# Performance work log

Hardware: AMD Instinct MI355X
Metric: run time of the kernel (lower is better)

## Reference

```python
import jax, jax.numpy as jnp
import numpy as np

N_NODES = 20000
N_EDGES = 320000
N_GRAPHS = 256
D = 256
L = 4
EPS = 1e-5


def setup_inputs() -> dict:
    key = jax.random.key(0)
    ks = jax.random.split(key, 20)
    x = jax.random.normal(ks[0], (N_NODES, D), dtype=jnp.float32)
    edge_index = jax.random.randint(ks[1], (2, N_EDGES), 0, N_NODES, dtype=jnp.int64)
    batch = jnp.sort(jax.random.randint(ks[2], (N_NODES,), 0, N_GRAPHS, dtype=jnp.int64))
    s = 1.0 / np.sqrt(D)
    Wl = jax.random.uniform(ks[3], (L, D, D), jnp.float32, -s, s)
    bl = jax.random.uniform(ks[4], (L, D), jnp.float32, -s, s)
    Wr = jax.random.uniform(ks[5], (L, D, D), jnp.float32, -s, s)
    gamma = jnp.ones((L, D), jnp.float32)
    beta = jnp.zeros((L, D), jnp.float32)
    fc1_w = jax.random.uniform(ks[6], (D, 128), jnp.float32, -s, s)
    fc1_b = jax.random.uniform(ks[7], (128,), jnp.float32, -s, s)
    s2 = 1.0 / np.sqrt(128)
    fc2_w = jax.random.uniform(ks[8], (128, 64), jnp.float32, -s2, s2)
    fc2_b = jax.random.uniform(ks[9], (64,), jnp.float32, -s2, s2)
    s3 = 1.0 / np.sqrt(64)
    fc3_w = jax.random.uniform(ks[10], (64, 10), jnp.float32, -s3, s3)
    fc3_b = jax.random.uniform(ks[11], (10,), jnp.float32, -s3, s3)
    return dict(x=x, edge_index=edge_index, batch=batch, Wl=Wl, bl=bl, Wr=Wr,
                gamma=gamma, beta=beta, fc1_w=fc1_w, fc1_b=fc1_b,
                fc2_w=fc2_w, fc2_b=fc2_b, fc3_w=fc3_w, fc3_b=fc3_b)


def reference(x, edge_index, batch, Wl, bl, Wr, gamma, beta,
              fc1_w, fc1_b, fc2_w, fc2_b, fc3_w, fc3_b):
    src, dst = edge_index[0], edge_index[1]
    # in-degree for mean aggregation (zero-degree nodes -> 0 aggregate)
    deg = jax.ops.segment_sum(jnp.ones((src.shape[0],), x.dtype), dst, num_segments=N_NODES)
    inv_deg = jnp.where(deg > 0, 1.0 / jnp.maximum(deg, 1.0), 0.0)[:, None]
    for i in range(L):
        # SAGEConv: mean-aggregate neighbors, then lin_l(agg) + lin_r(x)
        agg = jax.ops.segment_sum(x[src], dst, num_segments=N_NODES) * inv_deg
        h = agg @ Wl[i] + bl[i] + x @ Wr[i]
        # BatchNorm (training mode: biased batch statistics over nodes)
        mu = jnp.mean(h, axis=0)
        var = jnp.mean(jnp.square(h - mu), axis=0)
        h = (h - mu) * jax.lax.rsqrt(var + EPS) * gamma[i] + beta[i]
        x = jax.nn.relu(h)
    # global_mean_pool over graphs
    cnt = jax.ops.segment_sum(jnp.ones((N_NODES,), x.dtype), batch, num_segments=N_GRAPHS)
    g = jax.ops.segment_sum(x, batch, num_segments=N_GRAPHS) / jnp.maximum(cnt, 1.0)[:, None]
    # MLP classifier: 256 -> 128 -> 64 -> 10
    g = jax.nn.relu(g @ fc1_w + fc1_b)
    g = jax.nn.relu(g @ fc2_w + fc2_b)
    return g @ fc3_w + fc3_b
```

## Files before the change

### kernel.cpp

```cpp
#include <hip/hip_runtime.h>
#include <hip/hip_bf16.h>

#define NN 20000
#define NE 320000
#define NG 256
#define DD 256
#define NL 4
#define NBKT 79
#define BM 80
#define NBLK 250

typedef __attribute__((ext_vector_type(8))) short short8;
typedef __attribute__((ext_vector_type(4))) float float4_t;

__device__ __forceinline__ int ld_idx(const int* __restrict__ p, int i, int f64) {
    return f64 ? p[2 * i] : p[i];
}

__device__ __forceinline__ float bf2f(ushort u) {
    return __uint_as_float(((unsigned)u) << 16);
}

__device__ __forceinline__ ushort f2bf(float f) {
    __hip_bfloat16 b = __float2bfloat16(f);
    return *(ushort*)&b;
}


__global__ void k_init(const int* __restrict__ ei, const int* __restrict__ batch,
                       const ushort* __restrict__ x, int* __restrict__ flags,
                       int* __restrict__ deg) {
    int gid = blockIdx.x * 256 + threadIdx.x;
    for (int i = gid; i < NN; i += gridDim.x * 256) deg[i] = 0;
    if (blockIdx.x == 0) {
        __shared__ int cnt0, cnt1, weird;
        int t = threadIdx.x;
        if (t == 0) { cnt0 = 0; cnt1 = 0; weird = 0; }
        __syncthreads();
        for (int tt = t; tt < 512; tt += 256) {
            if (ei[2 * tt + 1] != 0) atomicAdd(&cnt0, 1);
            int i = tt * 9;
            if (batch[2 * i + 1] != 0) atomicAdd(&cnt1, 1);
#pragma unroll
            for (int j = 0; j < 16; j++) {
                ushort v = x[tt * 16 + j];
                if (((v >> 7) & 0xFF) >= 0xC0) atomicAdd(&weird, 1);
            }
        }
        __syncthreads();
        if (t == 0) {
            flags[0] = (cnt0 == 0) ? 1 : 0;
            flags[1] = (cnt1 == 0) ? 1 : 0;
            flags[2] = (weird == 0) ? 1 : 0;
        }
    }
}


#define POFF_BL   0
#define POFF_GA   1024
#define POFF_BE   2048
#define POFF_F1W  3072
#define POFF_F1B  35840
#define POFF_F2W  35968
#define POFF_F2B  44160
#define POFF_F3W  44224
#define POFF_F3B  44864
#define PTOT      44874

#define NB_CVT8   2500
#define NB_FRAG   128
#define NB_CVTP   176
#define NB_DEG    1250
#define NB_GST    79
#define B_FRAG    (NB_CVT8)
#define B_CVTP    (B_FRAG + NB_FRAG)
#define B_DEG     (B_CVTP + NB_CVTP)
#define B_GST     (B_DEG + NB_DEG)
#define NB_PREP   (B_GST + NB_GST)


__global__ __launch_bounds__(256) void k_prep(
    const void* __restrict__ x_in, const void* __restrict__ WL,
    const void* __restrict__ WR, const int* __restrict__ ei,
    const int* __restrict__ batch,
    const void* s0, const void* s1, const void* s2, const void* s3,
    const void* s4, const void* s5, const void* s6, const void* s7, const void* s8,
    ushort* __restrict__ xcan, ushort* __restrict__ wtL, ushort* __restrict__ wtR,
    ushort* __restrict__ pcan, int* __restrict__ deg, int* __restrict__ gstart,
    const int* __restrict__ fl) {
    int blk = blockIdx.x;
    int t = threadIdx.x;
    if (blk < B_FRAG) {
        int i = blk * 256 + t;
        if (fl[2]) {
            *(int4*)(xcan + (size_t)i * 8) = ((const int4*)x_in)[i];
        } else {
            const float* f = (const float*)x_in + (size_t)i * 8;
            ushort ov[8];
#pragma unroll
            for (int d = 0; d < 8; d++) ov[d] = f2bf(f[d]);
            *(int4*)(xcan + (size_t)i * 8) = *(int4*)ov;
        }
    } else if (blk < B_CVTP) {
        __shared__ ushort T[64][65];
        int bid = blk - B_FRAG;
        int lm = bid >> 4;
        int tile = bid & 15;
        int tk = (tile >> 2) * 64, tn = (tile & 3) * 64;
        const void* W = (lm >= 4) ? WR : WL;
        ushort* Wt = (lm >= 4) ? wtR : wtL;
        size_t base = (size_t)(lm & 3) << 16;
        int f32 = !fl[2];
#pragma unroll
        for (int i = 0; i < 16; i++) {
            int flat = t + i * 256;
            int r = flat >> 6, c = flat & 63;
            size_t src = base + (size_t)(tk + r) * 256 + tn + c;
            ushort v = f32 ? f2bf(((const float*)W)[src]) : ((const ushort*)W)[src];
            T[c][r] = v;
        }
        __syncthreads();
#pragma unroll
        for (int i = 0; i < 2; i++) {
            int slot = t + i * 256;
            int f = slot >> 6;
            int lane = slot & 63;
            int ln = (f >> 1) * 16 + (lane & 15);
            int lk = (f & 1) * 32 + ((lane >> 4) << 3);
            int gfblk = ((tn + ln) >> 4) * 8 + ((tk + lk) >> 5);
            ushort tmp[8];
#pragma unroll
            for (int j = 0; j < 8; j++) tmp[j] = T[ln][lk + j];
            *(int4*)(Wt + base + (size_t)gfblk * 512 + lane * 8) = *(int4*)tmp;
        }
    } else if (blk < B_DEG) {
        int i = (blk - B_CVTP) * 256 + t;
        if (i >= PTOT) return;
        const int offs[10] = {POFF_BL, POFF_GA, POFF_BE, POFF_F1W, POFF_F1B,
                              POFF_F2W, POFF_F2B, POFF_F3W, POFF_F3B, PTOT};
        const void* srcs[9] = {s0, s1, s2, s3, s4, s5, s6, s7, s8};
        int seg = 0;
#pragma unroll
        for (int k = 1; k < 9; k++) if (i >= offs[k]) seg = k;
        int local = i - offs[seg];
        if (fl[2]) pcan[i] = ((const ushort*)srcs[seg])[local];
        else       pcan[i] = f2bf(((const float*)srcs[seg])[local]);
    } else if (blk < B_GST) {
        int e = (blk - B_DEG) * 256 + t;
        if (e < NE) {
            int src = ld_idx(ei, e, fl[0]);
            int dst = ld_idx(ei, NE + e, fl[0]);
            if ((unsigned)dst < NN && (unsigned)src < NN) atomicAdd(&deg[dst], 1);
        }
    } else {
        int i = (blk - B_GST) * 256 + t;
        if (i >= NN) return;
        int b = ld_idx(batch, i, fl[1]);
        int bp = (i == 0) ? -1 : ld_idx(batch, i - 1, fl[1]);
        for (int g = bp + 1; g <= b; g++)
            if ((unsigned)g <= NG) gstart[g] = i;
        if (i == NN - 1)
            for (int g = b + 1; g <= NG; g++) gstart[g] = NN;
    }
}


__global__ __launch_bounds__(256) void k_scan(
    const int* __restrict__ deg, int* __restrict__ rowst,
    int* __restrict__ cursor, float* __restrict__ invdeg) {
    __shared__ int red[256];
    __shared__ int part[256];
    int b = blockIdx.x, t = threadIdx.x;
    int s = 0;
    for (int i = t; i < b * 256; i += 256) s += deg[i];
    red[t] = s;
    __syncthreads();
    for (int off = 128; off; off >>= 1) {
        if (t < off) red[t] += red[t + off];
        __syncthreads();
    }
    int bpref = red[0];
    int node = b * 256 + t;
    int d = (node < NN) ? deg[node] : 0;
    part[t] = d;
    __syncthreads();
    for (int off = 1; off < 256; off <<= 1) {
        int v = (t >= off) ? part[t - off] : 0;
        __syncthreads();
        part[t] += v;
        __syncthreads();
    }
    if (node < NN) {
        int o = bpref + part[t] - d;
        rowst[node] = o;
        cursor[node] = o;
        invdeg[node] = d > 0 ? 1.0f / (float)d : 0.0f;
    }
    if (b == NBKT - 1 && t == 255) rowst[NN] = bpref + part[255];
}

__global__ void k_fill(const int* __restrict__ ei, int* __restrict__ cursor,
                       int* __restrict__ csr, const int* __restrict__ fl) {
    int e = blockIdx.x * 256 + threadIdx.x;
    if (e < NE) {
        int src = ld_idx(ei, e, fl[0]);
        int dst = ld_idx(ei, NE + e, fl[0]);
        if ((unsigned)dst < NN && (unsigned)src < NN) {
            int p = atomicAdd(&cursor[dst], 1);
            if ((unsigned)p < NE) csr[p] = src;
        }
    }
}


template <int BNF>
__global__ __launch_bounds__(256) void k_agg4(
    const ushort* __restrict__ X, const int* __restrict__ rs,
    const int* __restrict__ csr, const float* __restrict__ invdeg,
    const float* __restrict__ bnsc, const float* __restrict__ bnsh,
    ushort* __restrict__ AGG) {
    int node = blockIdx.x * 4 + (threadIdx.x >> 6);
    if (node >= NN) return;
    int h = (threadIdx.x >> 5) & 1;
    int j = threadIdx.x & 31;
    float sc[8], sh[8];
    if (BNF) {
        float4 a0 = *(const float4*)(bnsc + j * 8);
        float4 a1 = *(const float4*)(bnsc + j * 8 + 4);
        float4 b0 = *(const float4*)(bnsh + j * 8);
        float4 b1 = *(const float4*)(bnsh + j * 8 + 4);
        sc[0] = a0.x; sc[1] = a0.y; sc[2] = a0.z; sc[3] = a0.w;
        sc[4] = a1.x; sc[5] = a1.y; sc[6] = a1.z; sc[7] = a1.w;
        sh[0] = b0.x; sh[1] = b0.y; sh[2] = b0.z; sh[3] = b0.w;
        sh[4] = b1.x; sh[5] = b1.y; sh[6] = b1.z; sh[7] = b1.w;
    }
    int e0 = rs[node], e1 = rs[node + 1];
    float acc[8] = {};
    int e = e0 + h;
    for (; e + 14 < e1; e += 16) {
        int4 v[8];
#pragma unroll
        for (int r = 0; r < 8; r++) {
            int s = csr[e + 2 * r];
            v[r] = *(const int4*)(X + (size_t)s * DD + j * 8);
        }
#pragma unroll
        for (int r = 0; r < 8; r++) {
            const ushort* u = (const ushort*)&v[r];
#pragma unroll
            for (int d = 0; d < 8; d++) {
                float x = bf2f(u[d]);
                if (BNF) x = fmaxf(x * sc[d] + sh[d], 0.0f);
                acc[d] += x;
            }
        }
    }
    for (; e + 2 < e1; e += 4) {
        int sA = csr[e], sB = csr[e + 2];
        int4 vA = *(const int4*)(X + (size_t)sA * DD + j * 8);
        int4 vB = *(const int4*)(X + (size_t)sB * DD + j * 8);
        const ushort* uA = (const ushort*)&vA;
        const ushort* uB = (const ushort*)&vB;
#pragma unroll
        for (int d = 0; d < 8; d++) {
            float xA = bf2f(uA[d]), xB = bf2f(uB[d]);
            if (BNF) {
                xA = fmaxf(xA * sc[d] + sh[d], 0.0f);
                xB = fmaxf(xB * sc[d] + sh[d], 0.0f);
            }
            acc[d] += xA + xB;
        }
    }
    for (; e < e1; e += 2) {
        int s = csr[e];
        int4 v = *(const int4*)(X + (size_t)s * DD + j * 8);
        const ushort* u = (const ushort*)&v;
#pragma unroll
        for (int d = 0; d < 8; d++) {
            float x = bf2f(u[d]);
            if (BNF) x = fmaxf(x * sc[d] + sh[d], 0.0f);
            acc[d] += x;
        }
    }
#pragma unroll
    for (int d = 0; d < 8; d++)
        acc[d] += __shfl_down(acc[d], 32);
    if (h == 0) {
        float inv = invdeg[node];
        ushort ov[8];
#pragma unroll
        for (int d = 0; d < 8; d++) ov[d] = f2bf(acc[d] * inv);
        *(int4*)(AGG + (size_t)node * DD + j * 8) = *(int4*)ov;
    }
}


template <int BNF>
__global__ __launch_bounds__(256) void k_gemm6(
    const ushort* __restrict__ A1, const ushort* __restrict__ A2,
    const ushort* __restrict__ WtF1, const ushort* __restrict__ WtF2,
    const ushort* __restrict__ bias,
    const float* __restrict__ bnsc, const float* __restrict__ bnsh,
    ushort* __restrict__ H, float* __restrict__ psumT, float* __restrict__ psqT) {
    __shared__ ushort Als[BM][264];
    __shared__ float colsum[128];
    __shared__ float colsq[128];
    const int m0 = blockIdx.x * BM;
    const int n0 = blockIdx.y * 128;
    const int tid = threadIdx.x;
    const int w = tid >> 6, lane = tid & 63;
    const int lr = lane & 15, q = lane >> 4;
    float4_t acc[5][2] = {};

    if (tid < 128) { colsum[tid] = 0.0f; colsq[tid] = 0.0f; }

    for (int mat = 0; mat < 2; ++mat) {
        const ushort* A = mat ? A2 : A1;
        const ushort* Wf = mat ? WtF2 : WtF1;
        __syncthreads();
#pragma unroll
        for (int i = 0; i < 10; i++) {
            int flat = tid + i * 256;
            int r = flat >> 5;
            int c = (flat & 31) * 8;
            int4 av = *(const int4*)(A + (size_t)(m0 + r) * DD + c);
            if (BNF && mat == 1) {
                ushort* u = (ushort*)&av;
#pragma unroll
                for (int d = 0; d < 8; d++)
                    u[d] = f2bf(fmaxf(bf2f(u[d]) * bnsc[c + d] + bnsh[c + d], 0.0f));
            }
            *(int4*)&Als[r][c] = av;
        }
        __syncthreads();
#pragma unroll
        for (int k0 = 0; k0 < 256; k0 += 32) {
            short8 af[5];
#pragma unroll
            for (int im = 0; im < 5; im++)
                af[im] = *(const short8*)&Als[im * 16 + lr][k0 + q * 8];
            const ushort* bbase =
                Wf + (((size_t)(((n0 + w * 32) >> 4) * 8 + (k0 >> 5))) << 9) + lane * 8;
#pragma unroll
            for (int in = 0; in < 2; in++) {
                short8 bf = *(const short8*)(bbase + in * 4096);
#pragma unroll
                for (int im = 0; im < 5; im++)
                    acc[im][in] = __builtin_amdgcn_mfma_f32_16x16x32_bf16(
                        af[im], bf, acc[im][in], 0, 0, 0);
            }
        }
    }

    const int mbase = m0 + q * 4;
#pragma unroll
    for (int in = 0; in < 2; ++in) {
        const int nl = w * 32 + in * 16 + lr;
        const int n = n0 + nl;
        float b = bf2f(bias[n]);
        float s = 0.0f, s2 = 0.0f;
#pragma unroll
        for (int im = 0; im < 5; ++im) {
#pragma unroll
            for (int i = 0; i < 4; ++i) {
                int m = mbase + im * 16 + i;
                float hv = acc[im][in][i] + b;
                ushort hb = f2bf(hv);
                H[(size_t)m * DD + n] = hb;
                float hq = bf2f(hb);
                s += hq;
                s2 += hq * hq;
            }
        }
        s += __shfl_xor(s, 16);  s += __shfl_xor(s, 32);
        s2 += __shfl_xor(s2, 16); s2 += __shfl_xor(s2, 32);
        if (q == 0) {
            atomicAdd(&colsum[nl], s);
            atomicAdd(&colsq[nl], s2);
        }
    }
    __syncthreads();
    if (tid < 128) {
        psumT[(size_t)(n0 + tid) * 256 + blockIdx.x] = colsum[tid];
        psqT[(size_t)(n0 + tid) * 256 + blockIdx.x] = colsq[tid];
    }
}


__global__ __launch_bounds__(64) void k_bnfinal3(
    const float* __restrict__ psumT, const float* __restrict__ psqT,
    const ushort* __restrict__ gamma, const ushort* __restrict__ beta,
    float* __restrict__ scale, float* __restrict__ shift) {
    int c = blockIdx.x;
    int t = threadIdx.x;
    float s = 0.0f, s2 = 0.0f;
    for (int b = t; b < NBLK; b += 64) {
        s += psumT[(size_t)c * 256 + b];
        s2 += psqT[(size_t)c * 256 + b];
    }
#pragma unroll
    for (int o = 32; o; o >>= 1) {
        s += __shfl_down(s, o);
        s2 += __shfl_down(s2, o);
    }
    if (t == 0) {
        float mu = s * (1.0f / NN);
        float var = s2 * (1.0f / NN) - mu * mu;
        if (var < 0.0f) var = 0.0f;
        float rstd = rsqrtf(var + 1e-5f);
        float g = bf2f(gamma[c]);
        float b2 = bf2f(beta[c]);
        scale[c] = g * rstd;
        shift[c] = b2 - mu * g * rstd;
    }
}


__global__ __launch_bounds__(256) void k_head(
    const ushort* __restrict__ Hb, const float* __restrict__ scale,
    const float* __restrict__ shift, const int* __restrict__ gstart,
    const ushort* __restrict__ fc1w, const ushort* __restrict__ fc1b,
    const ushort* __restrict__ fc2w, const ushort* __restrict__ fc2b,
    const ushort* __restrict__ fc3w, const ushort* __restrict__ fc3b,
    void* __restrict__ out, const int* __restrict__ fl) {
    __shared__ float g[256];
    __shared__ float h1[128];
    __shared__ float h2[64];
    __shared__ ushort w1[256 * 128];
    __shared__ ushort w2[128 * 64];
    __shared__ ushort w3[64 * 10];
    int gid = blockIdx.x;
    int t = threadIdx.x;
    for (int i = t; i < 256 * 128 / 8; i += 256) ((int4*)w1)[i] = ((const int4*)fc1w)[i];
    for (int i = t; i < 128 * 64 / 8; i += 256) ((int4*)w2)[i] = ((const int4*)fc2w)[i];
    if (t < 80) ((int4*)w3)[t] = ((const int4*)fc3w)[t];

    int s0 = gstart[gid], e = gstart[gid + 1];
    float sc = scale[t], sh = shift[t];
    float acc = 0.0f;
    int i = s0;
    for (; i + 7 < e; i += 8) {
        float v[8];
#pragma unroll
        for (int r = 0; r < 8; r++) v[r] = bf2f(Hb[(size_t)(i + r) * DD + t]);
#pragma unroll
        for (int r = 0; r < 8; r++) acc += fmaxf(v[r] * sc + sh, 0.0f);
    }
    for (; i < e; i++)
        acc += fmaxf(bf2f(Hb[(size_t)i * DD + t]) * sc + sh, 0.0f);
    g[t] = acc / fmaxf((float)(e - s0), 1.0f);
    __syncthreads();
    if (t < 128) {
        float a = bf2f(fc1b[t]);
#pragma unroll 8
        for (int k = 0; k < 256; k++)
            a += g[k] * bf2f(w1[k * 128 + t]);
        h1[t] = fmaxf(a, 0.0f);
    }
    __syncthreads();
    if (t < 64) {
        float a2 = bf2f(fc2b[t]);
#pragma unroll 8
        for (int k = 0; k < 128; k++)
            a2 += h1[k] * bf2f(w2[k * 64 + t]);
        h2[t] = fmaxf(a2, 0.0f);
    }
    __syncthreads();
    if (t < 10) {
        float a3 = bf2f(fc3b[t]);
#pragma unroll 8
        for (int k = 0; k < 64; k++)
            a3 += h2[k] * bf2f(w3[k * 10 + t]);
        if (fl[2]) ((__hip_bfloat16*)out)[gid * 10 + t] = __float2bfloat16(a3);
        else       ((float*)out)[gid * 10 + t] = a3;
    }
}


static inline char* bump(char*& p, size_t n) {
    char* r = p;
    p += (n + 255) & ~(size_t)255;
    return r;
}

extern "C" void kernel_launch(void* const* d_in, const int* in_sizes, int n_in,
                              void* d_out, int out_size, void* d_ws, size_t ws_size,
                              hipStream_t stream) {
    const void* x_in  = d_in[0];
    const int*  ei    = (const int*)d_in[1];
    const int*  batch = (const int*)d_in[2];
    const void* Wl    = d_in[3];
    const void* bl    = d_in[4];
    const void* Wr    = d_in[5];
    const void* gamma = d_in[6];
    const void* beta  = d_in[7];

    char* p = (char*)d_ws;
    int*    flags    = (int*)bump(p, 256);
    ushort* wtL      = (ushort*)bump(p, (size_t)NL * 65536 * 2);
    ushort* wtR      = (ushort*)bump(p, (size_t)NL * 65536 * 2);
    ushort* xcan     = (ushort*)bump(p, (size_t)NN * DD * 2);
    ushort* pcan     = (ushort*)bump(p, (size_t)PTOT * 2);
    int*    deg      = (int*)bump(p, NN * 4);
    int*    rowst    = (int*)bump(p, (NN + 1) * 4);
    int*    cursor   = (int*)bump(p, NN * 4);
    float*  invdeg   = (float*)bump(p, NN * 4);
    int*    csr      = (int*)bump(p, NE * 4);
    int*    gstart   = (int*)bump(p, (NG + 1) * 4);
    ushort* agg      = (ushort*)bump(p, (size_t)NN * DD * 2);
    ushort* hb0      = (ushort*)bump(p, (size_t)NN * DD * 2);
    ushort* hb1      = (ushort*)bump(p, (size_t)NN * DD * 2);
    float*  psumT    = (float*)bump(p, (size_t)DD * 256 * 4);
    float*  psqT     = (float*)bump(p, (size_t)DD * 256 * 4);
    float*  scale    = (float*)bump(p, DD * 4);
    float*  shift    = (float*)bump(p, DD * 4);

    if ((size_t)(p - (char*)d_ws) > ws_size) return;

    ushort* blc = pcan + POFF_BL;
    ushort* gac = pcan + POFF_GA;
    ushort* bec = pcan + POFF_BE;
    ushort* f1w = pcan + POFF_F1W;
    ushort* f1b = pcan + POFF_F1B;
    ushort* f2w = pcan + POFF_F2W;
    ushort* f2b = pcan + POFF_F2B;
    ushort* f3w = pcan + POFF_F3W;
    ushort* f3b = pcan + POFF_F3B;

    k_init<<<80, 256, 0, stream>>>(ei, batch, (const ushort*)x_in, flags, deg);
    k_prep<<<NB_PREP, 256, 0, stream>>>(
        x_in, Wl, Wr, ei, batch,
        bl, gamma, beta, d_in[8], d_in[9], d_in[10], d_in[11], d_in[12], d_in[13],
        xcan, wtL, wtR, pcan, deg, gstart, flags);
    k_scan<<<NBKT, 256, 0, stream>>>(deg, rowst, cursor, invdeg);
    k_fill<<<(NE + 255) / 256, 256, 0, stream>>>(ei, cursor, csr, flags);

    ushort* hbuf[2] = {hb0, hb1};
    const ushort* xsrc = xcan;
    for (int l = 0; l < NL; l++) {
        ushort* hdst = hbuf[l & 1];
        const ushort* wl = wtL + (size_t)l * 65536;
        const ushort* wr = wtR + (size_t)l * 65536;
        if (l == 0) {
            k_agg4<0><<<(NN + 3) / 4, 256, 0, stream>>>(xsrc, rowst, csr, invdeg,
                                                        scale, shift, agg);
            k_gemm6<0><<<dim3(NBLK, 2), 256, 0, stream>>>(
                agg, xsrc, wl, wr, blc, scale, shift, hdst, psumT, psqT);
        } else {
            k_agg4<1><<<(NN + 3) / 4, 256, 0, stream>>>(xsrc, rowst, csr, invdeg,
                                                        scale, shift, agg);
            k_gemm6<1><<<dim3(NBLK, 2), 256, 0, stream>>>(
                agg, xsrc, wl, wr, blc + l * DD, scale, shift, hdst, psumT, psqT);
        }
        k_bnfinal3<<<DD, 64, 0, stream>>>(psumT, psqT, gac + l * DD, bec + l * DD,
                                          scale, shift);
        xsrc = hdst;
    }

    k_head<<<NG, 256, 0, stream>>>(xsrc, scale, shift, gstart,
                                   f1w, f1b, f2w, f2b, f3w, f3b, d_out, flags);
}
```

Baseline: 357.2 us.

## Sort nodes by degree and split aggregation feature dims across blocks

Builds a degree histogram during the scan and a counting-sort permutation of nodes by in-degree in an extra fill block. The aggregation kernel now has each block handle 32 degree-sorted nodes for one 32-column slice of the feature dimension, with 8 blocks covering all 256 columns. The aim is to balance per-wavefront work by grouping nodes of similar degree and to improve cache locality of the gathered columns. In exchange, each node's CSR row is read 8 times and each gather load covers only 64 bytes of a source row.

```diff
diff --git a/kernel.cpp b/kernel.cpp
--- a/kernel.cpp
+++ b/kernel.cpp
@@ -9,6 +9,8 @@
 #define NBKT 79
 #define BM 80
 #define NBLK 250
+#define NCHK 625
+#define NB_FILL 1250
 
 typedef __attribute__((ext_vector_type(8))) short short8;
 typedef __attribute__((ext_vector_type(4))) float float4_t;
@@ -29,9 +31,10 @@
 
 __global__ void k_init(const int* __restrict__ ei, const int* __restrict__ batch,
                        const ushort* __restrict__ x, int* __restrict__ flags,
-                       int* __restrict__ deg) {
+                       int* __restrict__ deg, int* __restrict__ hist) {
     int gid = blockIdx.x * 256 + threadIdx.x;
     for (int i = gid; i < NN; i += gridDim.x * 256) deg[i] = 0;
+    if (gid < 256) hist[gid] = 0;
     if (blockIdx.x == 0) {
         __shared__ int cnt0, cnt1, weird;
         int t = threadIdx.x;
@@ -168,10 +171,13 @@
 
 __global__ __launch_bounds__(256) void k_scan(
     const int* __restrict__ deg, int* __restrict__ rowst,
-    int* __restrict__ cursor, float* __restrict__ invdeg) {
+    int* __restrict__ cursor, float* __restrict__ invdeg,
+    int* __restrict__ hist) {
     __shared__ int red[256];
     __shared__ int part[256];
+    __shared__ int lhist[256];
     int b = blockIdx.x, t = threadIdx.x;
+    lhist[t] = 0;
     int s = 0;
     for (int i = t; i < b * 256; i += 256) s += deg[i];
     red[t] = s;
@@ -196,40 +202,75 @@
         rowst[node] = o;
         cursor[node] = o;
         invdeg[node] = d > 0 ? 1.0f / (float)d : 0.0f;
+        atomicAdd(&lhist[d < 255 ? d : 255], 1);
     }
     if (b == NBKT - 1 && t == 255) rowst[NN] = bpref + part[255];
-}
+    __syncthreads();
+    atomicAdd(&hist[t], lhist[t]);
+}
+
 
 __global__ void k_fill(const int* __restrict__ ei, int* __restrict__ cursor,
-                       int* __restrict__ csr, const int* __restrict__ fl) {
-    int e = blockIdx.x * 256 + threadIdx.x;
-    if (e < NE) {
-        int src = ld_idx(ei, e, fl[0]);
-        int dst = ld_idx(ei, NE + e, fl[0]);
-        if ((unsigned)dst < NN && (unsigned)src < NN) {
-            int p = atomicAdd(&cursor[dst], 1);
-            if ((unsigned)p < NE) csr[p] = src;
-        }
+                       int* __restrict__ csr, const int* __restrict__ fl,
+                       const int* __restrict__ deg, const int* __restrict__ hist,
+                       int* __restrict__ order) {
+    if (blockIdx.x < NB_FILL) {
+        int e = blockIdx.x * 256 + threadIdx.x;
+        if (e < NE) {
+            int src = ld_idx(ei, e, fl[0]);
+            int dst = ld_idx(ei, NE + e, fl[0]);
+            if ((unsigned)dst < NN && (unsigned)src < NN) {
+                int p = atomicAdd(&cursor[dst], 1);
+                if ((unsigned)p < NE) csr[p] = src;
+            }
+        }
+        return;
+    }
+    __shared__ int curs[256];
+    int t = threadIdx.x;
+    int h = hist[t];
+    curs[t] = h;
+    __syncthreads();
+    for (int off = 1; off < 256; off <<= 1) {
+        int v = (t >= off) ? curs[t - off] : 0;
+        __syncthreads();
+        curs[t] += v;
+        __syncthreads();
+    }
+    int excl = curs[t] - h;
+    __syncthreads();
+    curs[t] = excl;
+    __syncthreads();
+    for (int i = t; i < NN; i += 256) {
+        int d = deg[i];
+        if (d > 255) d = 255;
+        int pos = atomicAdd(&curs[d], 1);
+        if ((unsigned)pos < NN) order[pos] = i;
     }
 }
 
 
 template <int BNF>
-__global__ __launch_bounds__(256) void k_agg4(
+__global__ __launch_bounds__(256) void k_agg5(
     const ushort* __restrict__ X, const int* __restrict__ rs,
     const int* __restrict__ csr, const float* __restrict__ invdeg,
     const float* __restrict__ bnsc, const float* __restrict__ bnsh,
-    ushort* __restrict__ AGG) {
-    int node = blockIdx.x * 4 + (threadIdx.x >> 6);
-    if (node >= NN) return;
-    int h = (threadIdx.x >> 5) & 1;
-    int j = threadIdx.x & 31;
+    const int* __restrict__ order, ushort* __restrict__ AGG) {
+    const int s = blockIdx.x & 7;
+    const int chunk = blockIdx.x >> 3;
+    const int tid = threadIdx.x;
+    const int w = tid >> 6, lane = tid & 63;
+    const int local = w * 8 + (lane >> 3);
+    const int h = (lane >> 2) & 1;
+    const int u = lane & 3;
+    const int db = s * 32 + u * 8;
+    const int node = order[chunk * 32 + local];
     float sc[8], sh[8];
     if (BNF) {
-        float4 a0 = *(const float4*)(bnsc + j * 8);
-        float4 a1 = *(const float4*)(bnsc + j * 8 + 4);
-        float4 b0 = *(const float4*)(bnsh + j * 8);
-        float4 b1 = *(const float4*)(bnsh + j * 8 + 4);
+        float4 a0 = *(const float4*)(bnsc + db);
+        float4 a1 = *(const float4*)(bnsc + db + 4);
+        float4 b0 = *(const float4*)(bnsh + db);
+        float4 b1 = *(const float4*)(bnsh + db + 4);
         sc[0] = a0.x; sc[1] = a0.y; sc[2] = a0.z; sc[3] = a0.w;
         sc[4] = a1.x; sc[5] = a1.y; sc[6] = a1.z; sc[7] = a1.w;
         sh[0] = b0.x; sh[1] = b0.y; sh[2] = b0.z; sh[3] = b0.w;
@@ -242,15 +283,15 @@
         int4 v[8];
 #pragma unroll
         for (int r = 0; r < 8; r++) {
-            int s = csr[e + 2 * r];
-            v[r] = *(const int4*)(X + (size_t)s * DD + j * 8);
+            int src = csr[e + 2 * r];
+            v[r] = *(const int4*)(X + (size_t)src * DD + db);
         }
 #pragma unroll
         for (int r = 0; r < 8; r++) {
-            const ushort* u = (const ushort*)&v[r];
+            const ushort* uu = (const ushort*)&v[r];
 #pragma unroll
             for (int d = 0; d < 8; d++) {
-                float x = bf2f(u[d]);
+                float x = bf2f(uu[d]);
                 if (BNF) x = fmaxf(x * sc[d] + sh[d], 0.0f);
                 acc[d] += x;
             }
@@ -258,8 +299,8 @@
     }
     for (; e + 2 < e1; e += 4) {
         int sA = csr[e], sB = csr[e + 2];
-        int4 vA = *(const int4*)(X + (size_t)sA * DD + j * 8);
-        int4 vB = *(const int4*)(X + (size_t)sB * DD + j * 8);
+        int4 vA = *(const int4*)(X + (size_t)sA * DD + db);
+        int4 vB = *(const int4*)(X + (size_t)sB * DD + db);
         const ushort* uA = (const ushort*)&vA;
         const ushort* uB = (const ushort*)&vB;
 #pragma unroll
@@ -273,25 +314,25 @@
         }
     }
     for (; e < e1; e += 2) {
-        int s = csr[e];
-        int4 v = *(const int4*)(X + (size_t)s * DD + j * 8);
-        const ushort* u = (const ushort*)&v;
+        int src = csr[e];
+        int4 v = *(const int4*)(X + (size_t)src * DD + db);
+        const ushort* uu = (const ushort*)&v;
 #pragma unroll
         for (int d = 0; d < 8; d++) {
-            float x = bf2f(u[d]);
+            float x = bf2f(uu[d]);
             if (BNF) x = fmaxf(x * sc[d] + sh[d], 0.0f);
             acc[d] += x;
         }
     }
 #pragma unroll
     for (int d = 0; d < 8; d++)
-        acc[d] += __shfl_down(acc[d], 32);
+        acc[d] += __shfl_down(acc[d], 4);
     if (h == 0) {
         float inv = invdeg[node];
         ushort ov[8];
 #pragma unroll
         for (int d = 0; d < 8; d++) ov[d] = f2bf(acc[d] * inv);
-        *(int4*)(AGG + (size_t)node * DD + j * 8) = *(int4*)ov;
+        *(int4*)(AGG + (size_t)node * DD + db) = *(int4*)ov;
     }
 }
 
@@ -498,6 +539,8 @@
 
     char* p = (char*)d_ws;
     int*    flags    = (int*)bump(p, 256);
+    int*    hist     = (int*)bump(p, 256 * 4);
+    int*    order    = (int*)bump(p, NN * 4);
     ushort* wtL      = (ushort*)bump(p, (size_t)NL * 65536 * 2);
     ushort* wtR      = (ushort*)bump(p, (size_t)NL * 65536 * 2);
     ushort* xcan     = (ushort*)bump(p, (size_t)NN * DD * 2);
@@ -528,13 +571,13 @@
     ushort* f3w = pcan + POFF_F3W;
     ushort* f3b = pcan + POFF_F3B;
 
-    k_init<<<80, 256, 0, stream>>>(ei, batch, (const ushort*)x_in, flags, deg);
+    k_init<<<80, 256, 0, stream>>>(ei, batch, (const ushort*)x_in, flags, deg, hist);
     k_prep<<<NB_PREP, 256, 0, stream>>>(
         x_in, Wl, Wr, ei, batch,
         bl, gamma, beta, d_in[8], d_in[9], d_in[10], d_in[11], d_in[12], d_in[13],
         xcan, wtL, wtR, pcan, deg, gstart, flags);
-    k_scan<<<NBKT, 256, 0, stream>>>(deg, rowst, cursor, invdeg);
-    k_fill<<<(NE + 255) / 256, 256, 0, stream>>>(ei, cursor, csr, flags);
+    k_scan<<<NBKT, 256, 0, stream>>>(deg, rowst, cursor, invdeg, hist);
+    k_fill<<<NB_FILL + 1, 256, 0, stream>>>(ei, cursor, csr, flags, deg, hist, order);
 
     ushort* hbuf[2] = {hb0, hb1};
     const ushort* xsrc = xcan;
@@ -543,13 +586,13 @@
         const ushort* wl = wtL + (size_t)l * 65536;
         const ushort* wr = wtR + (size_t)l * 65536;
         if (l == 0) {
-            k_agg4<0><<<(NN + 3) / 4, 256, 0, stream>>>(xsrc, rowst, csr, invdeg,
-                                                        scale, shift, agg);
+            k_agg5<0><<<NCHK * 8, 256, 0, stream>>>(xsrc, rowst, csr, invdeg,
+                                                    scale, shift, order, agg);
             k_gemm6<0><<<dim3(NBLK, 2), 256, 0, stream>>>(
                 agg, xsrc, wl, wr, blc, scale, shift, hdst, psumT, psqT);
         } else {
-            k_agg4<1><<<(NN + 3) / 4, 256, 0, stream>>>(xsrc, rowst, csr, invdeg,
-                                                        scale, shift, agg);
+            k_agg5<1><<<NCHK * 8, 256, 0, stream>>>(xsrc, rowst, csr, invdeg,
+                                                    scale, shift, order, agg);
             k_gemm6<1><<<dim3(NBLK, 2), 256, 0, stream>>>(
                 agg, xsrc, wl, wr, blc + l * DD, scale, shift, hdst, psumT, psqT);
         }
```

After: 396.6 us. 1.11x slower.
